# Kernel optimization log

Hardware: AMD Instinct MI355X
Metric: run time of the kernel (lower is better)

The kernel has to match this reference:

```python
import jax, jax.numpy as jnp
import numpy as np

N = 100000
E = 1600000
F_IN = 128
H = 128
NUM_GRAPHS = 512
EPS = 1e-5


def setup_inputs() -> dict:
    key = jax.random.key(0)
    ks = jax.random.split(key, 16)
    x = jax.random.normal(ks[0], (N, F_IN), dtype=jnp.float32)
    edge_index = jax.random.randint(ks[1], (2, E), 0, N, dtype=jnp.int32)
    batch = jnp.sort(jax.random.randint(ks[2], (N,), 0, NUM_GRAPHS, dtype=jnp.int32))
    def lin(k, fi, fo):
        s = 1.0 / np.sqrt(fi)
        return jax.random.uniform(k, (fi, fo), jnp.float32, -s, s)
    return {
        "x": x, "edge_index": edge_index, "batch": batch,
        "W1": lin(ks[3], F_IN, H), "b1": jnp.zeros((H,), jnp.float32),
        "g1": jnp.ones((H,), jnp.float32), "beta1": jnp.zeros((H,), jnp.float32),
        "W2": lin(ks[4], H, H), "b2": jnp.zeros((H,), jnp.float32),
        "g2": jnp.ones((H,), jnp.float32), "beta2": jnp.zeros((H,), jnp.float32),
        "W3": lin(ks[5], H, H), "b3": jnp.zeros((H,), jnp.float32),
        "g3": jnp.ones((H,), jnp.float32), "beta3": jnp.zeros((H,), jnp.float32),
        "Wl": lin(ks[6], H, 1), "bl": jnp.zeros((1,), jnp.float32),
    }


def _layer_norm(x, g, b):
    mu = jnp.mean(x, axis=-1, keepdims=True)
    var = jnp.mean((x - mu) ** 2, axis=-1, keepdims=True)
    return (x - mu) * jax.lax.rsqrt(var + EPS) * g + b


def _gcn_conv(x, W, b, src, dst, dinv):
    # GCNConv: D^{-1/2}(A+I)D^{-1/2} X W + b, deg includes self-loops
    h = x @ W                                   # [N,H]
    enorm = dinv[src] * dinv[dst]               # [E]
    agg = jax.ops.segment_sum(h[src] * enorm[:, None], dst, num_segments=N)
    agg = agg + h * (dinv * dinv)[:, None]      # self-loop contribution
    return agg + b


def reference(x, edge_index, batch, W1, b1, g1, beta1, W2, b2, g2, beta2,
              W3, b3, g3, beta3, Wl, bl):
    src, dst = edge_index[0], edge_index[1]
    deg = 1.0 + jax.ops.segment_sum(jnp.ones((E,), jnp.float32), dst, num_segments=N)
    dinv = jax.lax.rsqrt(deg)
    h = jax.nn.relu(_layer_norm(_gcn_conv(x, W1, b1, src, dst, dinv), g1, beta1))
    h = jax.nn.relu(_layer_norm(_gcn_conv(h, W2, b2, src, dst, dinv), g2, beta2))
    h = jax.nn.relu(_layer_norm(_gcn_conv(h, W3, b3, src, dst, dinv), g3, beta3))
    # global mean pool over graphs
    sums = jax.ops.segment_sum(h, batch, num_segments=NUM_GRAPHS)
    cnts = jax.ops.segment_sum(jnp.ones((N,), jnp.float32), batch, num_segments=NUM_GRAPHS)
    pooled = sums / jnp.maximum(cnts, 1.0)[:, None]
    return pooled @ Wl + bl                     # [NUM_GRAPHS, 1]
```

## Files before the change

kernel.cpp:

```cpp
#include <hip/hip_runtime.h>
#include <hip/hip_bf16.h>
#include <math.h>

#define N_NODES    100000
#define N_EDGES    1600000
#define FDIM       128
#define NUM_GRAPHS 512
#define EPS        1e-5f
#define PADN       100096

#define B_CVT   12512
#define B_WPK   192

#define NBUCK   196
#define CAPA    10240
#define EB_CHUNK 2048
#define BINA_BLOCKS ((N_EDGES + EB_CHUNK - 1) / EB_CHUNK)

typedef __attribute__((ext_vector_type(8))) __bf16 bf16x8;
typedef __attribute__((ext_vector_type(4))) float  f32x4;

__device__ __forceinline__ unsigned short f2bf(float f) {
    unsigned u = __builtin_bit_cast(unsigned, f);
    u += 0x7FFF + ((u >> 16) & 1);
    return (unsigned short)(u >> 16);
}
__device__ __forceinline__ float bf2f(unsigned short b) {
    unsigned u = ((unsigned)b) << 16;
    return __builtin_bit_cast(float, u);
}

__device__ __forceinline__ void dec4(unsigned dw, float* o) {
    auto lo = __builtin_amdgcn_cvt_pk_f32_fp8(dw, false);
    auto hi = __builtin_amdgcn_cvt_pk_f32_fp8(dw, true);
    o[0] = lo[0]; o[1] = lo[1]; o[2] = hi[0]; o[3] = hi[1];
}

__device__ __forceinline__ void acc16(uint4 v, float* a) {
    float d[16];
    dec4(v.x, &d[0]); dec4(v.y, &d[4]); dec4(v.z, &d[8]); dec4(v.w, &d[12]);
#pragma unroll
    for (int f = 0; f < 16; f++) a[f] += d[f];
}


__global__ __launch_bounds__(256) void k_build(const int* __restrict__ src,
                                               const int* __restrict__ dst,
                                               int* __restrict__ bcur,
                                               unsigned* __restrict__ binned,
                                               const float* __restrict__ x,
                                               unsigned short* __restrict__ xb,
                                               const float* __restrict__ W1,
                                               const float* __restrict__ W2,
                                               const float* __restrict__ W3,
                                               unsigned short* __restrict__ wp) {
    int b = blockIdx.x;
    int t = threadIdx.x;
    if (b < BINA_BLOCKS) {
        __shared__ int hist[NBUCK];
        __shared__ int lbase[NBUCK];
        __shared__ int loff[NBUCK];
        __shared__ unsigned lpack[EB_CHUNK];
        __shared__ unsigned short lbuck[EB_CHUNK];
        int e0 = b * EB_CHUNK;
        int nE = min(EB_CHUNK, N_EDGES - e0);

        for (int j = t; j < NBUCK; j += 256) { hist[j] = 0; loff[j] = 0; }
        __syncthreads();

        for (int k = t; k < nE; k += 256) {
            int e  = e0 + k;
            int d  = dst[e];
            int bk = d >> 9;
            lpack[k] = (unsigned)src[e] | ((unsigned)(d & 511) << 17);
            lbuck[k] = (unsigned short)bk;
            atomicAdd(&hist[bk], 1);
        }
        __syncthreads();
        for (int j = t; j < NBUCK; j += 256)
            lbase[j] = atomicAdd(&bcur[j], hist[j]);
        __syncthreads();

        for (int k = t; k < nE; k += 256) {
            int bk = lbuck[k];
            int p  = lbase[bk] + atomicAdd(&loff[bk], 1);
            binned[(size_t)bk * CAPA + p] = lpack[k];
        }
    } else if (b < BINA_BLOCKS + B_CVT) {
        long long idx = ((long long)(b - BINA_BLOCKS) * 256 + t) * 4;
        ushort4 o;
        if (idx < (long long)N_NODES * FDIM) {
            float4 v = *(const float4*)(x + idx);
            o.x = f2bf(v.x); o.y = f2bf(v.y); o.z = f2bf(v.z); o.w = f2bf(v.w);
        } else {
            o.x = o.y = o.z = o.w = 0;
        }
        *(ushort4*)(xb + idx) = o;
    } else {
        int wb  = b - (BINA_BLOCKS + B_CVT);
        int mat = wb >> 6;
        const float* W = (mat == 0) ? W1 : (mat == 1) ? W2 : W3;
        unsigned short* o = wp + (size_t)mat * 16384;
        int idx = (wb & 63) * 256 + t;
        int j  = idx & 7;
        int l  = (idx >> 3) & 63;
        int ct = (idx >> 9) & 7;
        int ks = idx >> 12;
        int k  = ks * 32 + (l >> 4) * 8 + j;
        int c  = ct * 16 + (l & 15);
        o[idx] = f2bf(W[k * 128 + c]);
    }
}


__global__ __launch_bounds__(256) void k_binB(const unsigned* __restrict__ binned,
                                              const int* __restrict__ bcur,
                                              int* __restrict__ offs,
                                              float* __restrict__ dinv,
                                              int* __restrict__ csr_src) {
    __shared__ int cnt_l[512];
    __shared__ int lofs[512];
    __shared__ int part[256];
    __shared__ int stage[CAPA];
    int b = blockIdx.x;
    int t = threadIdx.x;
    int nb0 = b * 512;
    int cnt = bcur[b];

    int pv = (t < b) ? bcur[t] : 0;
#pragma unroll
    for (int off = 32; off; off >>= 1) pv += __shfl_down(pv, off);
    part[t >> 6] = pv;
    __syncthreads();
    int seg0 = part[0];
    if (t == 0) {
    }
    __syncthreads();
    if ((t & 63) == 0) part[t >> 6] = pv;
    __syncthreads();
    seg0 = part[0] + part[1] + part[2] + part[3];

    cnt_l[t] = 0; cnt_l[t + 256] = 0;
    __syncthreads();

    for (int k = t; k < cnt; k += 256)
        atomicAdd(&cnt_l[binned[(size_t)b * CAPA + k] >> 17], 1);
    __syncthreads();

    int c0 = cnt_l[2 * t], c1 = cnt_l[2 * t + 1];
    int ps = c0 + c1;
    part[t] = ps;
    __syncthreads();
    for (int off = 1; off < 256; off <<= 1) {
        int y = 0;
        if (t >= off) y = part[t - off];
        __syncthreads();
        if (t >= off) part[t] += y;
        __syncthreads();
    }
    int excl = part[t] - ps;
    lofs[2 * t]     = excl;
    lofs[2 * t + 1] = excl + c0;
    __syncthreads();

    for (int j = t; j < 512; j += 256) {
        int node = nb0 + j;
        if (node < N_NODES) {
            offs[node] = seg0 + lofs[j];
            dinv[node] = rsqrtf(1.0f + (float)cnt_l[j]);
        }
    }
    if (b == NBUCK - 1 && t == 0) offs[N_NODES] = N_EDGES;
    __syncthreads();

    for (int k = t; k < cnt; k += 256) {
        unsigned v = binned[(size_t)b * CAPA + k];
        int ld = v >> 17;
        int p  = atomicAdd(&lofs[ld], 1);
        stage[p] = (int)(v & 0x1FFFF);
    }
    __syncthreads();
    for (int k = t; k < cnt; k += 256) csr_src[seg0 + k] = stage[k];
}


__global__ __launch_bounds__(256) void k_gemm(const unsigned short* __restrict__ A,
                                              const unsigned short* __restrict__ Wp,
                                              const float* __restrict__ dinv,
                                              unsigned char* __restrict__ C8) {
    int t    = threadIdx.x;
    int lane = t & 63;
    int w    = t >> 6;
    int wc   = w & 1;
    int wr   = w >> 1;
    int rb   = blockIdx.x * 128 + wr * 64 + (lane & 15);
    int koff = (lane >> 4) * 8;

    f32x4 acc[4][4];
#pragma unroll
    for (int c = 0; c < 4; c++)
#pragma unroll
        for (int r = 0; r < 4; r++) acc[c][r] = (f32x4){0.f, 0.f, 0.f, 0.f};

    const bf16x8* Wv = (const bf16x8*)Wp;
#pragma unroll
    for (int ks = 0; ks < 4; ++ks) {
        bf16x8 fw[4], fa[4];
#pragma unroll
        for (int c = 0; c < 4; ++c)
            fw[c] = Wv[(ks * 8 + wc * 4 + c) * 64 + lane];
#pragma unroll
        for (int r = 0; r < 4; ++r) {
            const uint4 v = *(const uint4*)(A + (size_t)(rb + r * 16) * 128 + ks * 32 + koff);
            fa[r] = __builtin_bit_cast(bf16x8, v);
        }
#pragma unroll
        for (int c = 0; c < 4; ++c)
#pragma unroll
            for (int r = 0; r < 4; ++r)
                acc[c][r] = __builtin_amdgcn_mfma_f32_16x16x32_bf16(fw[c], fa[r], acc[c][r], 0, 0, 0);
    }

#pragma unroll
    for (int r = 0; r < 4; ++r) {
        int row = blockIdx.x * 128 + wr * 64 + r * 16 + (lane & 15);
        if (row < N_NODES) {
            float dv = dinv[row];
#pragma unroll
            for (int c = 0; c < 4; ++c) {
                int col = (wc * 4 + c) * 16 + (lane >> 4) * 4;
                unsigned u = __builtin_amdgcn_cvt_pk_fp8_f32(acc[c][r][0] * dv, acc[c][r][1] * dv, 0, false);
                u = (unsigned)__builtin_amdgcn_cvt_pk_fp8_f32(acc[c][r][2] * dv, acc[c][r][3] * dv, (int)u, true);
                *(unsigned*)(C8 + (size_t)row * 128 + col) = u;
            }
        }
    }
}


__global__ __launch_bounds__(256) void k_agg(const unsigned char* __restrict__ h8,
                                             unsigned short* __restrict__ out,
                                             const int* __restrict__ offs,
                                             const int* __restrict__ csr_src,
                                             const float* __restrict__ dinv,
                                             const float* __restrict__ bias,
                                             const float* __restrict__ gamma,
                                             const float* __restrict__ beta) {
    int t    = threadIdx.x;
    int lane = t & 63;
    int grp  = lane >> 3;
    int sl   = lane & 7;
    int i    = blockIdx.x * 32 + (t >> 6) * 8 + grp;

    float di = dinv[i];
    size_t lofs16 = (size_t)sl * 16;

    float a[16];
    {
        uint4 v = *(const uint4*)(h8 + (size_t)i * 128 + lofs16);
        float d[16];
        dec4(v.x, &d[0]); dec4(v.y, &d[4]); dec4(v.z, &d[8]); dec4(v.w, &d[12]);
#pragma unroll
        for (int f = 0; f < 16; f++) a[f] = d[f];
    }

    int e0 = offs[i], e1 = offs[i + 1];
    int e = e0;
    for (; e + 8 <= e1; e += 8) {
        int s0 = csr_src[e + 0];
        int s1 = csr_src[e + 1];
        int s2 = csr_src[e + 2];
        int s3 = csr_src[e + 3];
        int s4 = csr_src[e + 4];
        int s5 = csr_src[e + 5];
        int s6 = csr_src[e + 6];
        int s7 = csr_src[e + 7];
        uint4 v0 = *(const uint4*)(h8 + (size_t)s0 * 128 + lofs16);
        uint4 v1 = *(const uint4*)(h8 + (size_t)s1 * 128 + lofs16);
        uint4 v2 = *(const uint4*)(h8 + (size_t)s2 * 128 + lofs16);
        uint4 v3 = *(const uint4*)(h8 + (size_t)s3 * 128 + lofs16);
        uint4 v4 = *(const uint4*)(h8 + (size_t)s4 * 128 + lofs16);
        uint4 v5 = *(const uint4*)(h8 + (size_t)s5 * 128 + lofs16);
        uint4 v6 = *(const uint4*)(h8 + (size_t)s6 * 128 + lofs16);
        uint4 v7 = *(const uint4*)(h8 + (size_t)s7 * 128 + lofs16);
        acc16(v0, a); acc16(v1, a); acc16(v2, a); acc16(v3, a);
        acc16(v4, a); acc16(v5, a); acc16(v6, a); acc16(v7, a);
    }
    for (; e + 4 <= e1; e += 4) {
        int s0 = csr_src[e + 0];
        int s1 = csr_src[e + 1];
        int s2 = csr_src[e + 2];
        int s3 = csr_src[e + 3];
        uint4 v0 = *(const uint4*)(h8 + (size_t)s0 * 128 + lofs16);
        uint4 v1 = *(const uint4*)(h8 + (size_t)s1 * 128 + lofs16);
        uint4 v2 = *(const uint4*)(h8 + (size_t)s2 * 128 + lofs16);
        uint4 v3 = *(const uint4*)(h8 + (size_t)s3 * 128 + lofs16);
        acc16(v0, a); acc16(v1, a); acc16(v2, a); acc16(v3, a);
    }
    for (; e < e1; ++e) {
        int s = csr_src[e];
        uint4 v = *(const uint4*)(h8 + (size_t)s * 128 + lofs16);
        acc16(v, a);
    }

    float4 b0 = *(const float4*)(bias + sl * 16);
    float4 b1 = *(const float4*)(bias + sl * 16 + 4);
    float4 b2 = *(const float4*)(bias + sl * 16 + 8);
    float4 b3 = *(const float4*)(bias + sl * 16 + 12);
    a[0]  = fmaf(a[0],  di, b0.x); a[1]  = fmaf(a[1],  di, b0.y);
    a[2]  = fmaf(a[2],  di, b0.z); a[3]  = fmaf(a[3],  di, b0.w);
    a[4]  = fmaf(a[4],  di, b1.x); a[5]  = fmaf(a[5],  di, b1.y);
    a[6]  = fmaf(a[6],  di, b1.z); a[7]  = fmaf(a[7],  di, b1.w);
    a[8]  = fmaf(a[8],  di, b2.x); a[9]  = fmaf(a[9],  di, b2.y);
    a[10] = fmaf(a[10], di, b2.z); a[11] = fmaf(a[11], di, b2.w);
    a[12] = fmaf(a[12], di, b3.x); a[13] = fmaf(a[13], di, b3.y);
    a[14] = fmaf(a[14], di, b3.z); a[15] = fmaf(a[15], di, b3.w);

    float s1 = 0.f, s2 = 0.f;
#pragma unroll
    for (int f = 0; f < 16; f++) { s1 += a[f]; s2 += a[f] * a[f]; }
#pragma unroll
    for (int off = 1; off < 8; off <<= 1) {
        s1 += __shfl_xor(s1, off);
        s2 += __shfl_xor(s2, off);
    }
    float mu   = s1 * (1.0f / 128.0f);
    float var  = s2 * (1.0f / 128.0f) - mu * mu;
    float rstd = rsqrtf(var + EPS);

    float g[16], be[16];
    {
        float4 g0 = *(const float4*)(gamma + sl * 16);
        float4 g1 = *(const float4*)(gamma + sl * 16 + 4);
        float4 g2 = *(const float4*)(gamma + sl * 16 + 8);
        float4 g3 = *(const float4*)(gamma + sl * 16 + 12);
        g[0]=g0.x; g[1]=g0.y; g[2]=g0.z; g[3]=g0.w;
        g[4]=g1.x; g[5]=g1.y; g[6]=g1.z; g[7]=g1.w;
        g[8]=g2.x; g[9]=g2.y; g[10]=g2.z; g[11]=g2.w;
        g[12]=g3.x; g[13]=g3.y; g[14]=g3.z; g[15]=g3.w;
        float4 e0v = *(const float4*)(beta + sl * 16);
        float4 e1v = *(const float4*)(beta + sl * 16 + 4);
        float4 e2v = *(const float4*)(beta + sl * 16 + 8);
        float4 e3v = *(const float4*)(beta + sl * 16 + 12);
        be[0]=e0v.x; be[1]=e0v.y; be[2]=e0v.z; be[3]=e0v.w;
        be[4]=e1v.x; be[5]=e1v.y; be[6]=e1v.z; be[7]=e1v.w;
        be[8]=e2v.x; be[9]=e2v.y; be[10]=e2v.z; be[11]=e2v.w;
        be[12]=e3v.x; be[13]=e3v.y; be[14]=e3v.z; be[15]=e3v.w;
    }

    unsigned ow[8];
#pragma unroll
    for (int f = 0; f < 8; f++) {
        float r0 = fmaxf((a[2*f]   - mu) * rstd * g[2*f]   + be[2*f],   0.f);
        float r1 = fmaxf((a[2*f+1] - mu) * rstd * g[2*f+1] + be[2*f+1], 0.f);
        ow[f] = (unsigned)f2bf(r0) | ((unsigned)f2bf(r1) << 16);
    }
    uint4* op = (uint4*)(out + (size_t)i * 128 + sl * 16);
    op[0] = make_uint4(ow[0], ow[1], ow[2], ow[3]);
    op[1] = make_uint4(ow[4], ow[5], ow[6], ow[7]);
}


__global__ __launch_bounds__(256) void k_pool(const unsigned short* __restrict__ h,
                                              const int* __restrict__ batch,
                                              const float* __restrict__ Wl,
                                              const float* __restrict__ bl,
                                              float* __restrict__ out) {
    __shared__ float2 part[4][64];
    int g = blockIdx.x;
    int t = threadIdx.x, w = t >> 6, lane = t & 63;

    int lo = 0, hi = N_NODES;
    while (lo < hi) { int mid = (lo + hi) >> 1; if (batch[mid] < g) lo = mid + 1; else hi = mid; }
    int s = lo;
    lo = s; hi = N_NODES;
    while (lo < hi) { int mid = (lo + hi) >> 1; if (batch[mid] < g + 1) lo = mid + 1; else hi = mid; }
    int e = lo;

    float ax = 0.f, ay = 0.f;
    for (int n = s + w; n < e; n += 4) {
        unsigned v = *(const unsigned*)(h + (size_t)n * 128 + lane * 2);
        ax += bf2f((unsigned short)(v & 0xffff));
        ay += bf2f((unsigned short)(v >> 16));
    }
    part[w][lane] = make_float2(ax, ay);
    __syncthreads();
    if (t < 64) {
        float sx = part[0][lane].x + part[1][lane].x + part[2][lane].x + part[3][lane].x;
        float sy = part[0][lane].y + part[1][lane].y + part[2][lane].y + part[3][lane].y;
        float cnt = fmaxf((float)(e - s), 1.0f);
        float inv = 1.0f / cnt;
        float p = sx * inv * Wl[lane * 2] + sy * inv * Wl[lane * 2 + 1];
#pragma unroll
        for (int off = 32; off; off >>= 1) p += __shfl_xor(p, off);
        if (lane == 0) out[g] = p + bl[0];
    }
}


extern "C" void kernel_launch(void* const* d_in, const int* in_sizes, int n_in,
                              void* d_out, int out_size, void* d_ws, size_t ws_size,
                              hipStream_t stream) {
    const float* x     = (const float*)d_in[0];
    const int*   ei    = (const int*)d_in[1];
    const int*   batch = (const int*)d_in[2];
    const float* W1 = (const float*)d_in[3];
    const float* b1 = (const float*)d_in[4];
    const float* g1 = (const float*)d_in[5];
    const float* be1 = (const float*)d_in[6];
    const float* W2 = (const float*)d_in[7];
    const float* b2 = (const float*)d_in[8];
    const float* g2 = (const float*)d_in[9];
    const float* be2 = (const float*)d_in[10];
    const float* W3 = (const float*)d_in[11];
    const float* b3 = (const float*)d_in[12];
    const float* g3 = (const float*)d_in[13];
    const float* be3 = (const float*)d_in[14];
    const float* Wl = (const float*)d_in[15];
    const float* bl = (const float*)d_in[16];

    const int* src = ei;
    const int* dst = ei + N_EDGES;

    char* ws = (char*)d_ws;
    size_t off = 0;
    auto alloc = [&](size_t bytes) -> void* {
        void* p = ws + off;
        off += (bytes + 255) & ~(size_t)255;
        return p;
    };
    unsigned short* xb   = (unsigned short*)alloc((size_t)PADN * FDIM * 2);
    unsigned short* hA   = (unsigned short*)alloc((size_t)PADN * FDIM * 2);
    unsigned char*  hF   = (unsigned char*)alloc((size_t)PADN * FDIM);
    unsigned short* wp   = (unsigned short*)alloc((size_t)3 * 16384 * 2);
    float* dinv    = (float*)alloc((size_t)N_NODES * 4);
    int*   offs    = (int*)alloc((size_t)(N_NODES + 1) * 4);
    int*   csr_src = (int*)alloc((size_t)N_EDGES * 4);
    unsigned* binned = (unsigned*)alloc((size_t)NBUCK * CAPA * 4);
    int*   bcur    = (int*)alloc(256 * 4);

    hipMemsetAsync(bcur, 0, 256 * 4, stream);

    k_build<<<BINA_BLOCKS + B_CVT + B_WPK, 256, 0, stream>>>(src, dst, bcur, binned,
                                                             x, xb, W1, W2, W3, wp);
    k_binB<<<NBUCK, 256, 0, stream>>>(binned, bcur, offs, dinv, csr_src);

    int gemm_grid = PADN / 128;
    int agg_grid  = N_NODES / 32;

    k_gemm<<<gemm_grid, 256, 0, stream>>>(xb, wp, dinv, hF);
    k_agg<<<agg_grid, 256, 0, stream>>>(hF, hA, offs, csr_src, dinv, b1, g1, be1);
    k_gemm<<<gemm_grid, 256, 0, stream>>>(hA, wp + 16384, dinv, hF);
    k_agg<<<agg_grid, 256, 0, stream>>>(hF, hA, offs, csr_src, dinv, b2, g2, be2);
    k_gemm<<<gemm_grid, 256, 0, stream>>>(hA, wp + 32768, dinv, hF);
    k_agg<<<agg_grid, 256, 0, stream>>>(hF, hA, offs, csr_src, dinv, b3, g3, be3);

    k_pool<<<NUM_GRAPHS, 256, 0, stream>>>(hA, batch, Wl, bl, (float*)d_out);
}
```

Baseline: 280.2 us.

## Sort CSR neighbors by source segment and software-pipeline index loads in aggregation

```diff
diff --git a/kernel.cpp b/kernel.cpp
--- a/kernel.cpp
+++ b/kernel.cpp
@@ -16,6 +16,8 @@
 #define CAPA    10240
 #define EB_CHUNK 2048
 #define BINA_BLOCKS ((N_EDGES + EB_CHUNK - 1) / EB_CHUNK)
+#define SEGSH   14
+#define SEGN    8
 
 typedef __attribute__((ext_vector_type(8))) __bf16 bf16x8;
 typedef __attribute__((ext_vector_type(4))) float  f32x4;
@@ -118,8 +120,8 @@
                                               int* __restrict__ offs,
                                               float* __restrict__ dinv,
                                               int* __restrict__ csr_src) {
-    __shared__ int cnt_l[512];
-    __shared__ int lofs[512];
+    __shared__ int cnt2[512 * SEGN];
+    __shared__ int lofs2[512 * SEGN];
     __shared__ int part[256];
     __shared__ int stage[CAPA];
     int b = blockIdx.x;
@@ -130,26 +132,28 @@
     int pv = (t < b) ? bcur[t] : 0;
 #pragma unroll
     for (int off = 32; off; off >>= 1) pv += __shfl_down(pv, off);
-    part[t >> 6] = pv;
-    __syncthreads();
-    int seg0 = part[0];
-    if (t == 0) {
-    }
-    __syncthreads();
     if ((t & 63) == 0) part[t >> 6] = pv;
     __syncthreads();
-    seg0 = part[0] + part[1] + part[2] + part[3];
-
-    cnt_l[t] = 0; cnt_l[t + 256] = 0;
-    __syncthreads();
-
-    for (int k = t; k < cnt; k += 256)
-        atomicAdd(&cnt_l[binned[(size_t)b * CAPA + k] >> 17], 1);
-    __syncthreads();
-
-    int c0 = cnt_l[2 * t], c1 = cnt_l[2 * t + 1];
-    int ps = c0 + c1;
-    part[t] = ps;
+    int seg0 = part[0] + part[1] + part[2] + part[3];
+    __syncthreads();
+
+    for (int j = t; j < 512 * SEGN; j += 256) cnt2[j] = 0;
+    __syncthreads();
+
+    for (int k = t; k < cnt; k += 256) {
+        unsigned v = binned[(size_t)b * CAPA + k];
+        int ld = v >> 17;
+        int s  = v & 0x1FFFF;
+        atomicAdd(&cnt2[ld * SEGN + (s >> SEGSH)], 1);
+    }
+    __syncthreads();
+
+    int base16 = t * 16;
+    int lsum[16];
+    int run = 0;
+#pragma unroll
+    for (int q = 0; q < 16; q++) { lsum[q] = run; run += cnt2[base16 + q]; }
+    part[t] = run;
     __syncthreads();
     for (int off = 1; off < 256; off <<= 1) {
         int y = 0;
@@ -158,16 +162,18 @@
         if (t >= off) part[t] += y;
         __syncthreads();
     }
-    int excl = part[t] - ps;
-    lofs[2 * t]     = excl;
-    lofs[2 * t + 1] = excl + c0;
+    int excl = part[t] - run;
+#pragma unroll
+    for (int q = 0; q < 16; q++) lofs2[base16 + q] = excl + lsum[q];
     __syncthreads();
 
     for (int j = t; j < 512; j += 256) {
         int node = nb0 + j;
         if (node < N_NODES) {
-            offs[node] = seg0 + lofs[j];
-            dinv[node] = rsqrtf(1.0f + (float)cnt_l[j]);
+            int st = lofs2[j * SEGN];
+            int en = (j == 511) ? cnt : lofs2[(j + 1) * SEGN];
+            offs[node] = seg0 + st;
+            dinv[node] = rsqrtf(1.0f + (float)(en - st));
         }
     }
     if (b == NBUCK - 1 && t == 0) offs[N_NODES] = N_EDGES;
@@ -176,8 +182,9 @@
     for (int k = t; k < cnt; k += 256) {
         unsigned v = binned[(size_t)b * CAPA + k];
         int ld = v >> 17;
-        int p  = atomicAdd(&lofs[ld], 1);
-        stage[p] = (int)(v & 0x1FFFF);
+        int s  = v & 0x1FFFF;
+        int p  = atomicAdd(&lofs2[ld * SEGN + (s >> SEGSH)], 1);
+        stage[p] = s;
     }
     __syncthreads();
     for (int k = t; k < cnt; k += 256) csr_src[seg0 + k] = stage[k];
@@ -264,40 +271,31 @@
         for (int f = 0; f < 16; f++) a[f] = d[f];
     }
 
-    int e0 = offs[i], e1 = offs[i + 1];
-    int e = e0;
-    for (; e + 8 <= e1; e += 8) {
-        int s0 = csr_src[e + 0];
-        int s1 = csr_src[e + 1];
-        int s2 = csr_src[e + 2];
-        int s3 = csr_src[e + 3];
-        int s4 = csr_src[e + 4];
-        int s5 = csr_src[e + 5];
-        int s6 = csr_src[e + 6];
-        int s7 = csr_src[e + 7];
+    int eBeg = offs[i], eEnd = offs[i + 1];
+    int e = eBeg;
+    int s0, s1, s2, s3;
+    if (e + 4 <= eEnd) {
+        s0 = csr_src[e + 0]; s1 = csr_src[e + 1];
+        s2 = csr_src[e + 2]; s3 = csr_src[e + 3];
+    }
+    for (; e + 8 <= eEnd; e += 4) {
         uint4 v0 = *(const uint4*)(h8 + (size_t)s0 * 128 + lofs16);
         uint4 v1 = *(const uint4*)(h8 + (size_t)s1 * 128 + lofs16);
         uint4 v2 = *(const uint4*)(h8 + (size_t)s2 * 128 + lofs16);
         uint4 v3 = *(const uint4*)(h8 + (size_t)s3 * 128 + lofs16);
-        uint4 v4 = *(const uint4*)(h8 + (size_t)s4 * 128 + lofs16);
-        uint4 v5 = *(const uint4*)(h8 + (size_t)s5 * 128 + lofs16);
-        uint4 v6 = *(const uint4*)(h8 + (size_t)s6 * 128 + lofs16);
-        uint4 v7 = *(const uint4*)(h8 + (size_t)s7 * 128 + lofs16);
+        s0 = csr_src[e + 4]; s1 = csr_src[e + 5];
+        s2 = csr_src[e + 6]; s3 = csr_src[e + 7];
         acc16(v0, a); acc16(v1, a); acc16(v2, a); acc16(v3, a);
-        acc16(v4, a); acc16(v5, a); acc16(v6, a); acc16(v7, a);
-    }
-    for (; e + 4 <= e1; e += 4) {
-        int s0 = csr_src[e + 0];
-        int s1 = csr_src[e + 1];
-        int s2 = csr_src[e + 2];
-        int s3 = csr_src[e + 3];
+    }
+    if (e + 4 <= eEnd) {
         uint4 v0 = *(const uint4*)(h8 + (size_t)s0 * 128 + lofs16);
         uint4 v1 = *(const uint4*)(h8 + (size_t)s1 * 128 + lofs16);
         uint4 v2 = *(const uint4*)(h8 + (size_t)s2 * 128 + lofs16);
         uint4 v3 = *(const uint4*)(h8 + (size_t)s3 * 128 + lofs16);
         acc16(v0, a); acc16(v1, a); acc16(v2, a); acc16(v3, a);
-    }
-    for (; e < e1; ++e) {
+        e += 4;
+    }
+    for (; e < eEnd; ++e) {
         int s = csr_src[e];
         uint4 v = *(const uint4*)(h8 + (size_t)s * 128 + lofs16);
         acc16(v, a);
@@ -316,16 +314,16 @@
     a[12] = fmaf(a[12], di, b3.x); a[13] = fmaf(a[13], di, b3.y);
     a[14] = fmaf(a[14], di, b3.z); a[15] = fmaf(a[15], di, b3.w);
 
-    float s1 = 0.f, s2 = 0.f;
-#pragma unroll
-    for (int f = 0; f < 16; f++) { s1 += a[f]; s2 += a[f] * a[f]; }
+    float s1v = 0.f, s2v = 0.f;
+#pragma unroll
+    for (int f = 0; f < 16; f++) { s1v += a[f]; s2v += a[f] * a[f]; }
 #pragma unroll
     for (int off = 1; off < 8; off <<= 1) {
-        s1 += __shfl_xor(s1, off);
-        s2 += __shfl_xor(s2, off);
-    }
-    float mu   = s1 * (1.0f / 128.0f);
-    float var  = s2 * (1.0f / 128.0f) - mu * mu;
+        s1v += __shfl_xor(s1v, off);
+        s2v += __shfl_xor(s2v, off);
+    }
+    float mu   = s1v * (1.0f / 128.0f);
+    float var  = s2v * (1.0f / 128.0f) - mu * mu;
     float rstd = rsqrtf(var + EPS);
 
     float g[16], be[16];
```

Result: faster. 263.8 us (-5.8%).
